# Kernel tuning notes

Hardware: AMD Instinct MI355X
Metric: run time of the kernel (lower is better)

Reference implementation:

```python
import jax, jax.numpy as jnp
import numpy as np

CUTOFF = 0.5


def setup_inputs() -> dict:
    key = jax.random.key(0)
    k_z, k_d, k_w, k_mu, k_sg = jax.random.split(key, 5)
    N, D_IN, D_OUT = 8192, 128, 128
    z = jax.random.normal(k_z, (N, D_IN), dtype=jnp.float32)
    dist_matrix = jax.random.uniform(k_d, (N, N), dtype=jnp.float32)
    W = jax.random.normal(k_w, (D_IN, D_OUT), dtype=jnp.float32)
    B = jnp.zeros((D_OUT,), dtype=jnp.float32)
    mu = jax.random.normal(k_mu, (1,), dtype=jnp.float32)
    sigma = jax.random.normal(k_sg, (1,), dtype=jnp.float32)
    return {"z": z, "dist_matrix": dist_matrix, "W": W, "B": B, "mu": mu, "sigma": sigma}


def reference(z, dist_matrix, W, B, mu, sigma):
    N = dist_matrix.shape[0]
    # transform every source node once: h[j] = z[j] @ W + B   [N, D_OUT]
    h = z @ W + B
    # pair mask: within cutoff and i != j
    mask = (dist_matrix < CUTOFF) & (~jnp.eye(N, dtype=bool))
    # safe distance to avoid inf/nan where masked out (original skips those pairs)
    r = jnp.where(mask, dist_matrix, 1.0)
    sens = jnp.exp(-(1.0 / r - 1.0 / mu[0]) ** 2 / (2.0 * sigma[0] ** 2))
    S = jnp.where(mask, sens, 0.0)  # [N, N]
    # z_inter[i] = sum_j S[i, j] * h[j]
    return S @ h
```

## Files before the change

kernel.cpp:

```cpp
#include <hip/hip_runtime.h>
#include <hip/hip_bf16.h>

#define NN 8192
#define DD 128
#define BM 16
#define JS 8
#define RPB 256
#define JSLICE 1024
#define JCHUNK 512
#define LSTR 1040

typedef __attribute__((ext_vector_type(4))) float f32x4;
typedef __attribute__((ext_vector_type(8))) short bf16x8;

__device__ __forceinline__ unsigned short f2bf(float x) {
    unsigned u = __float_as_uint(x);
    u += 0x7fffu + ((u >> 16) & 1u);
    return (unsigned short)(u >> 16);
}

__global__ void __launch_bounds__(256) h_transform(
    const float* __restrict__ z, const float* __restrict__ W,
    const float* __restrict__ Bv, unsigned short* __restrict__ hT) {
    __shared__ float zs[BM * DD];
    __shared__ float wt[DD * 132];
    const int t = threadIdx.x;
    const int j0 = blockIdx.x * BM;

    {
        const f32x4* zsrc = (const f32x4*)(z + (size_t)j0 * DD);
        f32x4* zdst = (f32x4*)zs;
        zdst[t] = zsrc[t];
        zdst[t + 256] = zsrc[t + 256];
    }
    for (int q = t; q < DD * 32; q += 256) {
        int k = q >> 5;
        int n0 = (q & 31) << 2;
        f32x4 wv = *(const f32x4*)(W + k * DD + n0);
        wt[(n0 + 0) * 132 + k] = wv[0];
        wt[(n0 + 1) * 132 + k] = wv[1];
        wt[(n0 + 2) * 132 + k] = wv[2];
        wt[(n0 + 3) * 132 + k] = wv[3];
    }
    __syncthreads();

    const int n = t >> 1;
    const int ja = (t & 1) << 3;
    float acc[8];
    float bn = Bv[n];
#pragma unroll
    for (int e = 0; e < 8; e++) acc[e] = bn;

#pragma unroll 8
    for (int k4 = 0; k4 < 32; ++k4) {
        f32x4 wv = *(const f32x4*)&wt[n * 132 + (k4 << 2)];
#pragma unroll
        for (int e = 0; e < 8; e++) {
            f32x4 zv = *(const f32x4*)&zs[(ja + e) * DD + (k4 << 2)];
            acc[e] += zv[0] * wv[0] + zv[1] * wv[1] + zv[2] * wv[2] + zv[3] * wv[3];
        }
    }

    const int j = j0 + ja;
    unsigned short* dst = hT + (size_t)n * NN + j;
    uint4 uv;
    uv.x = (unsigned)f2bf(acc[0]) | ((unsigned)f2bf(acc[1]) << 16);
    uv.y = (unsigned)f2bf(acc[2]) | ((unsigned)f2bf(acc[3]) << 16);
    uv.z = (unsigned)f2bf(acc[4]) | ((unsigned)f2bf(acc[5]) << 16);
    uv.w = (unsigned)f2bf(acc[6]) | ((unsigned)f2bf(acc[7]) << 16);
    *(uint4*)dst = uv;
}

__device__ __forceinline__ bf16x8 sfrag(f32x4 a, f32x4 b, int jbase, int diag,
                                        float inv_mu, float ninv2s2) {
    float v0[4] = {a[0], a[1], a[2], a[3]};
    float v1[4] = {b[0], b[1], b[2], b[3]};
    unsigned short h[8];
#pragma unroll
    for (int e = 0; e < 4; ++e) {
        float d = v0[e];
        float q = __builtin_amdgcn_rcpf(d) - inv_mu;
        float s = __expf(q * q * ninv2s2);
        bool keep = (d < 0.5f) & ((jbase + e) != diag);
        h[e] = f2bf(keep ? s : 0.0f);
    }
#pragma unroll
    for (int e = 0; e < 4; ++e) {
        float d = v1[e];
        float q = __builtin_amdgcn_rcpf(d) - inv_mu;
        float s = __expf(q * q * ninv2s2);
        bool keep = (d < 0.5f) & ((jbase + 4 + e) != diag);
        h[4 + e] = f2bf(keep ? s : 0.0f);
    }
    uint4 u;
    u.x = (unsigned)h[0] | ((unsigned)h[1] << 16);
    u.y = (unsigned)h[2] | ((unsigned)h[3] << 16);
    u.z = (unsigned)h[4] | ((unsigned)h[5] << 16);
    u.w = (unsigned)h[6] | ((unsigned)h[7] << 16);
    return __builtin_bit_cast(bf16x8, u);
}

__global__ void __launch_bounds__(512, 2) fused_interact(
    const float* __restrict__ dist, const unsigned short* __restrict__ hT,
    const float* __restrict__ mu, const float* __restrict__ sigma,
    float* __restrict__ part) {
    __shared__ uint4 hs4[DD * (LSTR / 16)];
    char* hs = (char*)hs4;

    const int t = threadIdx.x;
    const int w = t >> 6;
    const int l = t & 63;
    const int rb = blockIdx.x >> 3;
    const int js = blockIdx.x & 7;
    const int r0 = rb * RPB + w * 32;
    const int row = l & 15;
    const int kc8 = (l >> 4) << 3;
    const int q16 = (l >> 4) << 4;

    const float inv_mu = 1.0f / mu[0];
    const float sg = sigma[0];
    const float ninv2s2 = -1.0f / (2.0f * sg * sg);

    const float* dp0 = dist + (size_t)(r0 + row) * NN + kc8;
    const float* dp1 = dp0 + (size_t)16 * NN;
    const int diag0 = r0 + row;
    const int diag1 = diag0 + 16;
    const char* hbase = hs + row * LSTR + q16;

    f32x4 acc[2][8];
#pragma unroll
    for (int m = 0; m < 2; ++m)
#pragma unroll
        for (int f = 0; f < 8; ++f) acc[m][f] = (f32x4){0.f, 0.f, 0.f, 0.f};

    f32x4 dA0a, dA0b, dA1a, dA1b, dB0a, dB0b, dB1a, dB1b;

#define LOADD(Da, Db, Dc, Dd, K)                                             \
    do {                                                                     \
        Da = *(const f32x4*)(dp0 + (K));                                     \
        Db = *(const f32x4*)(dp0 + (K) + 4);                                 \
        Dc = *(const f32x4*)(dp1 + (K));                                     \
        Dd = *(const f32x4*)(dp1 + (K) + 4);                                 \
    } while (0)

#define COMPUTE(Da, Db, Dc, Dd, K, LK)                                       \
    do {                                                                     \
        bf16x8 a0 = sfrag(Da, Db, (K) + kc8, diag0, inv_mu, ninv2s2);        \
        bf16x8 a1 = sfrag(Dc, Dd, (K) + kc8, diag1, inv_mu, ninv2s2);        \
        _Pragma("unroll") for (int f = 0; f < 8; ++f) {                      \
            bf16x8 bb = *(const bf16x8*)(hbase + f * (16 * LSTR) + (LK));    \
            acc[0][f] = __builtin_amdgcn_mfma_f32_16x16x32_bf16(             \
                a0, bb, acc[0][f], 0, 0, 0);                                 \
            acc[1][f] = __builtin_amdgcn_mfma_f32_16x16x32_bf16(             \
                a1, bb, acc[1][f], 0, 0, 0);                                 \
        }                                                                    \
    } while (0)

#pragma unroll 1
    for (int chunk = 0; chunk < 2; ++chunk) {
        const int jc = js * JSLICE + chunk * JCHUNK;
        __syncthreads();
        {
            uint4 tmp[16];
#pragma unroll
            for (int i = 0; i < 16; ++i) {
                int c = i * 512 + t;
                int n = c >> 6;
                int cb = c & 63;
                tmp[i] = *(const uint4*)(hT + (size_t)n * NN + jc + cb * 8);
            }
#pragma unroll
            for (int i = 0; i < 16; ++i) {
                int c = i * 512 + t;
                int n = c >> 6;
                int cb = c & 63;
                *(uint4*)(hs + n * LSTR + cb * 16) = tmp[i];
            }
        }
        __syncthreads();

        LOADD(dA0a, dA0b, dA1a, dA1b, jc);
        LOADD(dB0a, dB0b, dB1a, dB1b, jc + 32);
#pragma unroll 1
        for (int it = 0; it < 16; it += 2) {
            const int kg = jc + (it << 5);
            const int lk = it << 6;
            COMPUTE(dA0a, dA0b, dA1a, dA1b, kg, lk);
            if (it + 2 < 16) LOADD(dA0a, dA0b, dA1a, dA1b, kg + 64);
            COMPUTE(dB0a, dB0b, dB1a, dB1b, kg + 32, lk + 64);
            if (it + 3 < 16) LOADD(dB0a, dB0b, dB1a, dB1b, kg + 96);
        }
    }

    float* po = part + (size_t)js * (NN * DD);
    const int orow = r0 + ((l >> 4) << 2);
    const int ocol = l & 15;
#pragma unroll
    for (int m = 0; m < 2; ++m)
#pragma unroll
        for (int f = 0; f < 8; ++f)
#pragma unroll
            for (int rr = 0; rr < 4; ++rr)
                po[(size_t)(orow + m * 16 + rr) * DD + f * 16 + ocol] =
                    acc[m][f][rr];
#undef LOADD
#undef COMPUTE
}

__global__ void __launch_bounds__(256) reduce_part(
    const float* __restrict__ part, float* __restrict__ outp) {
    const size_t idx = ((size_t)blockIdx.x * 256 + threadIdx.x) << 2;
    f32x4 s = *(const f32x4*)(part + idx);
#pragma unroll
    for (int ksp = 1; ksp < JS; ++ksp)
        s += *(const f32x4*)(part + (size_t)ksp * (NN * DD) + idx);
    *(f32x4*)(outp + idx) = s;
}

extern "C" void kernel_launch(void* const* d_in, const int* in_sizes, int n_in,
                              void* d_out, int out_size, void* d_ws, size_t ws_size,
                              hipStream_t stream) {
    const float* z = (const float*)d_in[0];
    const float* dist = (const float*)d_in[1];
    const float* W = (const float*)d_in[2];
    const float* Bv = (const float*)d_in[3];
    const float* mu = (const float*)d_in[4];
    const float* sigma = (const float*)d_in[5];
    float* out = (float*)d_out;

    unsigned short* hT = (unsigned short*)d_ws;
    const size_t hT_bytes = (size_t)DD * NN * 2;
    float* part = (float*)((char*)d_ws + hT_bytes);

    h_transform<<<NN / BM, 256, 0, stream>>>(z, W, Bv, hT);
    fused_interact<<<(NN / RPB) * JS, 512, 0, stream>>>(dist, hT, mu, sigma,
                                                        part);
    reduce_part<<<(NN * DD) / 1024, 256, 0, stream>>>(part, out);
}
```

Measured before the change: 108.6 us.

## Stage sensitivity tile in LDS with coalesced dist loads and smaller row blocks

Restructures the fused interaction kernel so each 128-column K block loads dist rows coalesced across threads, computes the masked Gaussian sensitivities once, and writes them as bf16 into an LDS tile. MFMA A-fragments are then read from that tile. Row blocks shrink from 256 to 128 rows, with one 16-row M tile per wave, and occupancy is raised to four blocks per CU. This trades register-resident, prefetched dist fragments for an extra LDS round trip and two barriers per K block, with no overlap between global loads and MFMA.

```diff
diff --git a/kernel.cpp b/kernel.cpp
--- a/kernel.cpp
+++ b/kernel.cpp
@@ -5,10 +5,10 @@
 #define DD 128
 #define BM 16
 #define JS 8
-#define RPB 256
+#define RPB 128
 #define JSLICE 1024
-#define JCHUNK 512
-#define LSTR 1040
+#define KBLK 128
+#define LSTR 272
 
 typedef __attribute__((ext_vector_type(4))) float f32x4;
 typedef __attribute__((ext_vector_type(8))) short bf16x8;
@@ -71,140 +71,99 @@
     *(uint4*)dst = uv;
 }
 
-__device__ __forceinline__ bf16x8 sfrag(f32x4 a, f32x4 b, int jbase, int diag,
-                                        float inv_mu, float ninv2s2) {
-    float v0[4] = {a[0], a[1], a[2], a[3]};
-    float v1[4] = {b[0], b[1], b[2], b[3]};
-    unsigned short h[8];
-#pragma unroll
-    for (int e = 0; e < 4; ++e) {
-        float d = v0[e];
-        float q = __builtin_amdgcn_rcpf(d) - inv_mu;
-        float s = __expf(q * q * ninv2s2);
-        bool keep = (d < 0.5f) & ((jbase + e) != diag);
-        h[e] = f2bf(keep ? s : 0.0f);
-    }
-#pragma unroll
-    for (int e = 0; e < 4; ++e) {
-        float d = v1[e];
-        float q = __builtin_amdgcn_rcpf(d) - inv_mu;
-        float s = __expf(q * q * ninv2s2);
-        bool keep = (d < 0.5f) & ((jbase + 4 + e) != diag);
-        h[4 + e] = f2bf(keep ? s : 0.0f);
-    }
-    uint4 u;
-    u.x = (unsigned)h[0] | ((unsigned)h[1] << 16);
-    u.y = (unsigned)h[2] | ((unsigned)h[3] << 16);
-    u.z = (unsigned)h[4] | ((unsigned)h[5] << 16);
-    u.w = (unsigned)h[6] | ((unsigned)h[7] << 16);
-    return __builtin_bit_cast(bf16x8, u);
-}
-
-__global__ void __launch_bounds__(512, 2) fused_interact(
+__global__ void __launch_bounds__(512, 4) fused_interact(
     const float* __restrict__ dist, const unsigned short* __restrict__ hT,
     const float* __restrict__ mu, const float* __restrict__ sigma,
     float* __restrict__ part) {
-    __shared__ uint4 hs4[DD * (LSTR / 16)];
-    char* hs = (char*)hs4;
+    __shared__ char s_lds[RPB * LSTR];
+    __shared__ char h_lds[DD * LSTR];
 
     const int t = threadIdx.x;
     const int w = t >> 6;
     const int l = t & 63;
-    const int rb = blockIdx.x >> 3;
-    const int js = blockIdx.x & 7;
-    const int r0 = rb * RPB + w * 32;
-    const int row = l & 15;
-    const int kc8 = (l >> 4) << 3;
-    const int q16 = (l >> 4) << 4;
+    const int rb = (int)blockIdx.x >> 3;
+    const int js = (int)blockIdx.x & 7;
+    const int r0 = rb * RPB;
+
+    const int dr = t >> 5;
+    const int dc = (t & 31) << 2;
+    const int hn = t >> 4;
+    const int hc = (t & 15) << 3;
+
+    const int fr = l & 15;
+    const int fq = l >> 4;
+    const int a_base = (w * 16 + fr) * LSTR + fq * 16;
+    const int b_base = fr * LSTR + fq * 16;
 
     const float inv_mu = 1.0f / mu[0];
     const float sg = sigma[0];
     const float ninv2s2 = -1.0f / (2.0f * sg * sg);
 
-    const float* dp0 = dist + (size_t)(r0 + row) * NN + kc8;
-    const float* dp1 = dp0 + (size_t)16 * NN;
-    const int diag0 = r0 + row;
-    const int diag1 = diag0 + 16;
-    const char* hbase = hs + row * LSTR + q16;
-
-    f32x4 acc[2][8];
+    f32x4 acc[8];
 #pragma unroll
-    for (int m = 0; m < 2; ++m)
-#pragma unroll
-        for (int f = 0; f < 8; ++f) acc[m][f] = (f32x4){0.f, 0.f, 0.f, 0.f};
-
-    f32x4 dA0a, dA0b, dA1a, dA1b, dB0a, dB0b, dB1a, dB1b;
-
-#define LOADD(Da, Db, Dc, Dd, K)                                             \
-    do {                                                                     \
-        Da = *(const f32x4*)(dp0 + (K));                                     \
-        Db = *(const f32x4*)(dp0 + (K) + 4);                                 \
-        Dc = *(const f32x4*)(dp1 + (K));                                     \
-        Dd = *(const f32x4*)(dp1 + (K) + 4);                                 \
-    } while (0)
-
-#define COMPUTE(Da, Db, Dc, Dd, K, LK)                                       \
-    do {                                                                     \
-        bf16x8 a0 = sfrag(Da, Db, (K) + kc8, diag0, inv_mu, ninv2s2);        \
-        bf16x8 a1 = sfrag(Dc, Dd, (K) + kc8, diag1, inv_mu, ninv2s2);        \
-        _Pragma("unroll") for (int f = 0; f < 8; ++f) {                      \
-            bf16x8 bb = *(const bf16x8*)(hbase + f * (16 * LSTR) + (LK));    \
-            acc[0][f] = __builtin_amdgcn_mfma_f32_16x16x32_bf16(             \
-                a0, bb, acc[0][f], 0, 0, 0);                                 \
-            acc[1][f] = __builtin_amdgcn_mfma_f32_16x16x32_bf16(             \
-                a1, bb, acc[1][f], 0, 0, 0);                                 \
-        }                                                                    \
-    } while (0)
+    for (int f = 0; f < 8; ++f) acc[f] = (f32x4){0.f, 0.f, 0.f, 0.f};
 
 #pragma unroll 1
-    for (int chunk = 0; chunk < 2; ++chunk) {
-        const int jc = js * JSLICE + chunk * JCHUNK;
-        __syncthreads();
-        {
-            uint4 tmp[16];
+    for (int chunk = 0; chunk < JSLICE / KBLK; ++chunk) {
+        const int jc = js * JSLICE + chunk * KBLK;
+
+        f32x4 dv[8];
+        uint4 hv[4];
 #pragma unroll
-            for (int i = 0; i < 16; ++i) {
-                int c = i * 512 + t;
-                int n = c >> 6;
-                int cb = c & 63;
-                tmp[i] = *(const uint4*)(hT + (size_t)n * NN + jc + cb * 8);
-            }
+        for (int p = 0; p < 8; ++p)
+            dv[p] = *(const f32x4*)(dist + (size_t)(r0 + p * 16 + dr) * NN +
+                                    jc + dc);
 #pragma unroll
-            for (int i = 0; i < 16; ++i) {
-                int c = i * 512 + t;
-                int n = c >> 6;
-                int cb = c & 63;
-                *(uint4*)(hs + n * LSTR + cb * 16) = tmp[i];
-            }
-        }
+        for (int q = 0; q < 4; ++q)
+            hv[q] = *(const uint4*)(hT + (size_t)(hn + q * 32) * NN + jc + hc);
+
         __syncthreads();
 
-        LOADD(dA0a, dA0b, dA1a, dA1b, jc);
-        LOADD(dB0a, dB0b, dB1a, dB1b, jc + 32);
-#pragma unroll 1
-        for (int it = 0; it < 16; it += 2) {
-            const int kg = jc + (it << 5);
-            const int lk = it << 6;
-            COMPUTE(dA0a, dA0b, dA1a, dA1b, kg, lk);
-            if (it + 2 < 16) LOADD(dA0a, dA0b, dA1a, dA1b, kg + 64);
-            COMPUTE(dB0a, dB0b, dB1a, dB1b, kg + 32, lk + 64);
-            if (it + 3 < 16) LOADD(dB0a, dB0b, dB1a, dB1b, kg + 96);
+#pragma unroll
+        for (int q = 0; q < 4; ++q)
+            *(uint4*)(h_lds + (hn + q * 32) * LSTR + (hc << 1)) = hv[q];
+
+#pragma unroll
+        for (int p = 0; p < 8; ++p) {
+            const int rloc = p * 16 + dr;
+            const int rg = r0 + rloc;
+            unsigned short h[4];
+#pragma unroll
+            for (int e = 0; e < 4; ++e) {
+                float d = dv[p][e];
+                float q = __builtin_amdgcn_rcpf(d) - inv_mu;
+                float s = __expf(q * q * ninv2s2);
+                bool keep = (d < 0.5f) & ((jc + dc + e) != rg);
+                h[e] = f2bf(keep ? s : 0.0f);
+            }
+            uint2 u;
+            u.x = (unsigned)h[0] | ((unsigned)h[1] << 16);
+            u.y = (unsigned)h[2] | ((unsigned)h[3] << 16);
+            *(uint2*)(s_lds + rloc * LSTR + (dc << 1)) = u;
+        }
+
+        __syncthreads();
+
+#pragma unroll
+        for (int ks = 0; ks < 4; ++ks) {
+            bf16x8 a = *(const bf16x8*)(s_lds + a_base + ks * 64);
+#pragma unroll
+            for (int f = 0; f < 8; ++f) {
+                bf16x8 b =
+                    *(const bf16x8*)(h_lds + b_base + f * (16 * LSTR) + ks * 64);
+                acc[f] = __builtin_amdgcn_mfma_f32_16x16x32_bf16(a, b, acc[f],
+                                                                 0, 0, 0);
+            }
         }
     }
 
     float* po = part + (size_t)js * (NN * DD);
-    const int orow = r0 + ((l >> 4) << 2);
-    const int ocol = l & 15;
+    const int orow = r0 + w * 16 + (fq << 2);
 #pragma unroll
-    for (int m = 0; m < 2; ++m)
+    for (int f = 0; f < 8; ++f)
 #pragma unroll
-        for (int f = 0; f < 8; ++f)
-#pragma unroll
-            for (int rr = 0; rr < 4; ++rr)
-                po[(size_t)(orow + m * 16 + rr) * DD + f * 16 + ocol] =
-                    acc[m][f][rr];
-#undef LOADD
-#undef COMPUTE
+        for (int rr = 0; rr < 4; ++rr)
+            po[(size_t)(orow + rr) * DD + f * 16 + fr] = acc[f][rr];
 }
 
 __global__ void __launch_bounds__(256) reduce_part(
```

Result: slower. 127.9 us (+17.7%).
